# Kernel tuning notes

Hardware: AMD Instinct MI355X
Metric: run time of the kernel (lower is better)

The kernel has to match this reference:

```python
import jax, jax.numpy as jnp
import numpy as np

B, T, D, M, HID = 8, 128, 512, 2048, 128
EPS = 1e-5

def layer_norm(x, g, b):
    mu = jnp.mean(x, axis=-1, keepdims=True)
    var = jnp.mean((x - mu) ** 2, axis=-1, keepdims=True)
    return (x - mu) * jax.lax.rsqrt(var + EPS) * g + b

def setup_inputs() -> dict:
    key = jax.random.key(0)
    ks = jax.random.split(key, 12)
    f32 = jnp.float32
    inp = {
        'e': jax.random.normal(ks[0], (B, T, D), f32),
        'h': jax.random.randint(ks[1], (D,), 0, M),
        'sign': (jax.random.randint(ks[2], (D,), 0, 2) * 2 - 1).astype(f32),
        'Wq': jax.random.normal(ks[3], (D, D), f32) / np.sqrt(D),
        'Wk': jax.random.normal(ks[4], (D, D), f32) / np.sqrt(D),
        'Wv': jax.random.normal(ks[5], (D, D), f32) / np.sqrt(D),
        'ro_w1': jax.random.normal(ks[6], (M, HID), f32) / np.sqrt(M),
        'ro_b1': jnp.zeros((HID,), f32),
        'ro_w2': jax.random.normal(ks[7], (HID, D), f32) / np.sqrt(HID),
        'ro_b2': jnp.zeros((D,), f32),
        'vp_ln_g': jnp.ones((D,), f32),
        'vp_ln_b': jnp.zeros((D,), f32),
        'vp_w1': jax.random.normal(ks[8], (D, D), f32) / np.sqrt(D),
        'vp_b1': jnp.zeros((D,), f32),
        'vp_w2': jax.random.normal(ks[9], (D, D), f32) / np.sqrt(D),
        'vp_b2': jnp.zeros((D,), f32),
        'ln_g': jnp.ones((D,), f32),
        'ln_b': jnp.zeros((D,), f32),
        'theta_q_raw': jnp.asarray(0.05, f32),
        'theta_k_raw': jnp.asarray(0.05, f32),
        'omega_raw': jnp.asarray(0.02, f32),
        'gate_feat_raw': jnp.asarray(-2.5, f32),
        'gate_val_raw': jnp.asarray(-2.5, f32),
    }
    return inp

def reference(e, h, sign, Wq, Wk, Wv, ro_w1, ro_b1, ro_w2, ro_b2,
              vp_ln_g, vp_ln_b, vp_w1, vp_b1, vp_w2, vp_b2, ln_g, ln_b,
              theta_q_raw, theta_k_raw, omega_raw, gate_feat_raw, gate_val_raw):
    sg = jax.lax.stop_gradient
    # CountSketch as a sparse signed projection matrix (d -> m), row i hits col h[i].
    CS = jnp.zeros((D, M), e.dtype).at[jnp.arange(D), h].set(sign)
    theta_q = 0.5 * jnp.tanh(theta_q_raw)
    theta_k = 0.5 * jnp.tanh(theta_k_raw)
    omega = 0.5 * jnp.tanh(omega_raw)
    g_feat = 0.25 * jax.nn.sigmoid(gate_feat_raw)  # gate_cap_feat=0.25
    g_val = 0.25 * jax.nn.sigmoid(gate_val_raw)    # gate_cap_val=0.25

    def step(carry, xs):
        K, H = carry              # K:(B,2,M)  H:(B,2,D,M)  (detached buffers)
        e_t, t = xs               # e_t:(B,D)  t: scalar position
        pos = jnp.full((e_t.shape[0], 1), t, e_t.dtype)
        q = e_t @ Wq
        k = e_t @ Wk
        v = e_t @ Wv
        ph_q = theta_q * q - omega * pos
        ph_k = theta_k * k + omega * pos
        Q_re = (q * jnp.cos(ph_q)) @ CS
        Q_im = (q * jnp.sin(ph_q)) @ CS
        dK_re = (k * jnp.cos(ph_k)) @ CS
        dK_im = (k * jnp.sin(ph_k)) @ CS
        # FFT polynomial convolution of query sketch with prefix-key sketch
        FQ = jnp.fft.fft(jax.lax.complex(Q_re, Q_im), norm='ortho')
        Kd = sg(K)
        FK = jnp.fft.fft(jax.lax.complex(Kd[:, 0, :], Kd[:, 1, :]), norm='ortho')
        tscale = jnp.sqrt(pos + 1.0)
        psi = jnp.fft.ifft(FQ * FK, norm='ortho').real / tscale
        h_feat = jax.nn.gelu(psi @ ro_w1 + ro_b1, approximate=False) @ ro_w2 + ro_b2
        # value readout against prefix H (reads are detached, as in torch)
        Hd = sg(H)
        vread = (jnp.einsum('bdm,bm->bd', Hd[:, 0], sg(Q_re))
                 - jnp.einsum('bdm,bm->bd', Hd[:, 1], sg(Q_im))) / tscale
        vread = layer_norm(vread, vp_ln_g, vp_ln_b)
        vread = jax.nn.gelu(vread @ vp_w1 + vp_b1, approximate=False) @ vp_w2 + vp_b2
        y = layer_norm(e_t + g_feat * h_feat + g_val * vread, ln_g, ln_b)
        dK = sg(jnp.stack([dK_re, dK_im], axis=1))        # (B,2,M)
        K_next = Kd + dK
        H_next = Hd + v[:, None, :, None] * dK[:, :, None, :]
        return (K_next, H_next), y

    K0 = jnp.zeros((B, 2, M), e.dtype)
    H0 = jnp.zeros((B, 2, D, M), e.dtype)
    pos_seq = jnp.arange(T, dtype=e.dtype)
    (Kf, Hf), ys = jax.lax.scan(step, (K0, H0), (jnp.transpose(e, (1, 0, 2)), pos_seq))
    return jnp.transpose(ys, (1, 0, 2)), Kf, Hf
```

## Files before the change

kernel.cpp:

```cpp
#include <hip/hip_runtime.h>
#include <hip/hip_bf16.h>
#include <math.h>

#define B_   8
#define T_   128
#define D_   512
#define M_   2048
#define HID_ 128
#define BT_  1024

typedef __attribute__((ext_vector_type(8))) short short8t;
typedef __attribute__((ext_vector_type(8))) unsigned short ushort8t;
typedef __attribute__((ext_vector_type(4))) unsigned short ushort4t;
typedef __attribute__((ext_vector_type(4))) float f32x4;
typedef __hip_bfloat16 bf16;

#define OFF_SCAL   0L
#define OFF_QKV    16L
#define OFF_KP     (OFF_QKV + 1572864L)
#define OFF_VRAW   (OFF_KP + 2097152L)
#define OFF_VF     (OFF_VRAW + 524288L)
#define OFF_HFEAT  (OFF_VF + 524288L)
#define OFF_EB     (OFF_HFEAT + 524288L)
#define OFF_WQKVT  (OFF_EB + 262144L)
#define OFF_VP1T   (OFF_WQKVT + 393216L)
#define OFF_VP2T   (OFF_VP1T + 131072L)
#define OFF_RO2T   (OFF_VP2T + 131072L)
#define OFF_QCAT   (OFF_RO2T + 32768L)
#define OFF_KCAT   (OFF_QCAT + 2097152L)
#define OFF_DKT    (OFF_KCAT + 2097152L)
#define OFF_VTB    (OFF_DKT + 2097152L)
#define OFF_VLNB   (OFF_VTB + 262144L)
#define OFF_V1B    (OFF_VLNB + 262144L)
#define OFF_SCOA   (OFF_V1B + 262144L)
#define OFF_QSUM   (OFF_SCOA + 131072L)
#define OFF_PCAT   (OFF_QSUM + 131072L)
#define OFF_RO1F   (OFF_PCAT + 2097152L)
#define OFF_HACC   (OFF_RO1F + 262144L)

#define FLAG_BIAS     1
#define FLAG_GELU     2
#define FLAG_ROWSCALE 4
#define FLAG_ATOMIC   8
#define FLAG_HFB      32
#define FLAG_TRI      64

__device__ __forceinline__ float gelu_f(float x) {
    return 0.5f * x * (1.0f + erff(x * 0.70710678118654752440f));
}

__device__ __forceinline__ float b2f(unsigned short u) {
    return __uint_as_float(((unsigned int)u) << 16);
}

#define PIDX(i) ((i) + ((i) >> 5))

template<int M>
__device__ __forceinline__ void dif_one(float* re, float* im, int tid) {
    #pragma unroll
    for (int u = 0; u < 4; ++u) {
        int q = u * 256 + tid;
        int k = q & (M - 1);
        int i = (q / M) * (2 * M) + k;
        float s, c;
        __sincosf((float)k * (3.14159265358979323846f / (float)M), &s, &c);
        int p0 = PIDX(i), p1 = PIDX(i + M);
        float ar = re[p0], ai = im[p0], br = re[p1], bi = im[p1];
        re[p0] = ar + br; im[p0] = ai + bi;
        float dr = ar - br, di = ai - bi;
        re[p1] = dr * c + di * s;
        im[p1] = di * c - dr * s;
    }
}

__global__ __launch_bounds__(256) void preproc_kernel(
    const float* tq, const float* tk, const float* om, const float* gf, const float* gv,
    float* scal, float* scoacc, float* hacc,
    const float4* __restrict__ e4, ushort4t* __restrict__ eb4,
    const float* w0, const float* w1, const float* w2, const float* w3,
    const float* w4, const float* w5,
    bf16* d0, bf16* d1, bf16* d2, bf16* d3, bf16* d4, bf16* d5,
    const float* __restrict__ ro_w1, bf16* __restrict__ ro1f)
{
    __shared__ float smem[4224];
    int blk = blockIdx.x, tid = threadIdx.x;

    if (blk < 1024) {
        int idx = blk * 256 + tid;
        if (idx < 131072) scoacc[idx] = 0.f;
        else hacc[idx - 131072] = 0.f;
        if (idx == 0) {
            scal[0] = 0.5f * tanhf(tq[0]);
            scal[1] = 0.5f * tanhf(tk[0]);
            scal[2] = 0.5f * tanhf(om[0]);
            scal[3] = 0.25f / (1.0f + expf(-gf[0]));
            scal[4] = 0.25f / (1.0f + expf(-gv[0]));
        }
        return;
    }
    if (blk < 1536) {
        int i = (blk - 1024) * 256 + tid;
        float4 v = e4[i];
        ushort4t o;
        bf16 h0 = __float2bfloat16(v.x), h1 = __float2bfloat16(v.y);
        bf16 h2 = __float2bfloat16(v.z), h3 = __float2bfloat16(v.w);
        o[0] = *(unsigned short*)&h0; o[1] = *(unsigned short*)&h1;
        o[2] = *(unsigned short*)&h2; o[3] = *(unsigned short*)&h3;
        eb4[i] = o;
        return;
    }
    if (blk < 3072) {
        int zz = blk - 1536;
        int wz = zz >> 8;
        int rem = zz & 255;
        int by = rem >> 4, bx = rem & 15;
        const float* src; bf16* dst; int R = 512;
        if (wz == 0)      { src = w0; dst = d0; }
        else if (wz == 1) { src = w1; dst = d1; }
        else if (wz == 2) { src = w2; dst = d2; }
        else if (wz == 3) { src = w3; dst = d3; }
        else if (wz == 4) { src = w4; dst = d4; }
        else              { src = w5; dst = d5; R = 128; }
        int c0 = bx * 32, r0 = by * 32;
        if (r0 >= R) return;
        float (*tile)[33] = (float(*)[33])smem;
        int tx = tid & 31, ty = tid >> 5;
        for (int rr = ty; rr < 32; rr += 8) {
            int r = r0 + rr;
            tile[rr][tx] = (r < R) ? src[(long)r * 512 + c0 + tx] : 0.f;
        }
        __syncthreads();
        int r = r0 + tx;
        if (r < R)
            for (int cc = ty; cc < 32; cc += 8)
                dst[(long)(c0 + cc) * R + r] = __float2bfloat16(tile[tx][cc]);
        return;
    }
    {
        int j = blk - 3072;
        float* Rs = smem;
        float* Is = smem + 2112;
        for (int u = 0; u < 8; ++u) {
            int n = u * 256 + tid;
            Rs[PIDX(n)] = ro_w1[(long)n * HID_ + j];
            Is[PIDX(n)] = 0.f;
        }
        __syncthreads();
#define FSTEP(MM) dif_one<MM>(Rs, Is, tid); __syncthreads();
        FSTEP(1024) FSTEP(512) FSTEP(256) FSTEP(128) FSTEP(64)
        FSTEP(32) FSTEP(16) FSTEP(8) FSTEP(4) FSTEP(2) FSTEP(1)
#undef FSTEP
        unsigned short* op = (unsigned short*)(ro1f + (long)j * 4096);
        for (int u = 0; u < 8; ++u) {
            int r = u * 256 + tid;
            int pr = PIDX(r);
            bf16 re = __float2bfloat16(Rs[pr]);
            bf16 im = __float2bfloat16(Is[pr]);
            op[r]        = *(unsigned short*)&re;
            op[2048 + r] = *(unsigned short*)&im;
        }
    }
}

__global__ __launch_bounds__(256) void sketchvtb_kernel(const float* __restrict__ qkv,
                                                        const float* __restrict__ sign,
                                                        const float* __restrict__ scal,
                                                        const int* __restrict__ h,
                                                        bf16* __restrict__ qcat,
                                                        bf16* __restrict__ kcat,
                                                        bf16* __restrict__ vTb) {
    __shared__ float smem[4 * M_];
    int blk = blockIdx.x, tid = threadIdx.x;
    if (blk < 1024) {
        int bt = blk;
        float* s0 = smem;
        float* s1 = smem + M_;
        float* s2 = smem + 2 * M_;
        float* s3 = smem + 3 * M_;
        for (int j = tid; j < M_; j += 256) { s0[j] = 0.f; s1[j] = 0.f; s2[j] = 0.f; s3[j] = 0.f; }
        __syncthreads();
        int t = bt & 127;
        float thq = scal[0], thk = scal[1], omg = scal[2];
        float ft = (float)t;
        for (int i = tid; i < D_; i += 256) {
            float q = qkv[(long)bt * 1536 + i];
            float k = qkv[(long)bt * 1536 + 512 + i];
            float sg = sign[i];
            float sq_, cq_, sk_, ck_;
            __sincosf(thq * q - omg * ft, &sq_, &cq_);
            __sincosf(thk * k + omg * ft, &sk_, &ck_);
            int m = h[i];
            atomicAdd(&s0[m], q * cq_ * sg);
            atomicAdd(&s1[m], q * sq_ * sg);
            atomicAdd(&s2[m], k * ck_ * sg);
            atomicAdd(&s3[m], k * sk_ * sg);
        }
        __syncthreads();
        long qb = (long)bt * 4096;
        for (int j = tid; j < M_; j += 256) {
            qcat[qb + j]        = __float2bfloat16(s0[j]);
            qcat[qb + 2048 + j] = __float2bfloat16(s1[j]);
            kcat[qb + j]        = __float2bfloat16(s2[j]);
            kcat[qb + 2048 + j] = __float2bfloat16(-s3[j]);
        }
        return;
    }
    {
        int zz = blk - 1024;
        int b = zz >> 6;
        int rem = zz & 63;
        int by = rem >> 4, bx = rem & 15;
        int c0 = bx * 32, r0 = by * 32;
        float (*tile)[33] = (float(*)[33])smem;
        int tx = tid & 31, ty = tid >> 5;
        const float* in = qkv + 1024 + (long)b * 196608L;
        for (int rr = ty; rr < 32; rr += 8)
            tile[rr][tx] = in[(long)(r0 + rr) * 1536 + c0 + tx];
        __syncthreads();
        bf16* out = vTb + (long)b * 65536L;
        for (int cc = ty; cc < 32; cc += 8)
            out[(long)(c0 + cc) * 128 + r0 + tx] = __float2bfloat16(tile[tx][cc]);
    }
}

__global__ __launch_bounds__(256) void prefix_p1(const bf16* __restrict__ kcat,
                                                 float* __restrict__ qsum) {
    int idx = blockIdx.x * 256 + threadIdx.x;
    int col = idx & 32767, q = idx >> 15;
    int m = col & 2047, b = (col >> 11) & 7, comp = col >> 14;
    const unsigned short* src = (const unsigned short*)kcat
        + ((long)(b * 128 + q * 32) * 4096L + (long)comp * 2048L + m);
    float s = 0.f;
    #pragma unroll 8
    for (int i = 0; i < 32; ++i) s += b2f(src[(long)i * 4096L]);
    if (comp) s = -s;
    qsum[(long)q * 32768 + col] = s;
}

__global__ __launch_bounds__(256) void prefix_p2(const bf16* __restrict__ kcat,
                                                 const float* __restrict__ qsum,
                                                 bf16* __restrict__ KP16,
                                                 bf16* __restrict__ dkT,
                                                 float* __restrict__ kf_out) {
    int idx = blockIdx.x * 256 + threadIdx.x;
    int col = idx & 32767, q = idx >> 15;
    int m = col & 2047, b = (col >> 11) & 7, comp = col >> 14;
    const unsigned short* src = (const unsigned short*)kcat
        + ((long)(b * 128 + q * 32) * 4096L + (long)comp * 2048L + m);
    bf16* dst = KP16 + (long)comp * BT_ * M_ + (long)b * T_ * M_ + m + (long)(q * 32) * M_;
    bf16* dkt = dkT + (long)comp * 2097152L + (long)b * 262144L + (long)m * 128L + (long)(q * 32);
    float acc = 0.f;
    for (int p = 0; p < q; ++p) acc += qsum[(long)p * 32768 + col];
    float sgn = comp ? -1.f : 1.f;
    #pragma unroll 4
    for (int i = 0; i < 32; ++i) {
        float v = sgn * b2f(src[(long)i * 4096L]);
        dst[(long)i * M_] = __float2bfloat16(acc);
        dkt[i] = __float2bfloat16(v);
        acc += v;
    }
    if (q == 3) kf_out[((long)b * 2 + comp) * M_ + m] = acc;
}

template<int S>
__device__ __forceinline__ void dif8_pair(float* r0, float* i0a, float* r1, float* i1a, int tid) {
    int k = tid % S;
    int grp = tid / S;
    int base = grp * 8 * S + k;
    float sw, cw;
    __sincosf((float)k * (3.14159265358979323846f / (4.0f * (float)S)), &sw, &cw);
    float wr = cw, wi = -sw;
    float w2r = wr * wr - wi * wi, w2i = 2.f * wr * wi;
    float w4r = w2r * w2r - w2i * w2i, w4i = 2.f * w2r * w2i;
    const float RH = 0.70710678118654752440f;
    float t1r[4] = {wr, (wr + wi) * RH, wi, (wi - wr) * RH};
    float t1i[4] = {wi, (wi - wr) * RH, -wr, -(wr + wi) * RH};
    float u0r = w2r, u0i = w2i;
    float u1r = w2i, u1i = -w2r;
    #pragma unroll
    for (int a = 0; a < 2; ++a) {
        float* re = a ? r1 : r0;
        float* im = a ? i1a : i0a;
        float xr[8], xi[8];
        #pragma unroll
        for (int r = 0; r < 8; ++r) { int p = PIDX(base + r * S); xr[r] = re[p]; xi[r] = im[p]; }
        #pragma unroll
        for (int r = 0; r < 4; ++r) {
            float ar = xr[r], ai = xi[r], br = xr[r + 4], bi = xi[r + 4];
            xr[r] = ar + br; xi[r] = ai + bi;
            float dr = ar - br, di = ai - bi;
            xr[r + 4] = dr * t1r[r] - di * t1i[r];
            xi[r + 4] = dr * t1i[r] + di * t1r[r];
        }
        #pragma unroll
        for (int hb = 0; hb < 8; hb += 4) {
            #pragma unroll
            for (int r = 0; r < 2; ++r) {
                float tr = (r == 0) ? u0r : u1r, ti = (r == 0) ? u0i : u1i;
                float ar = xr[hb + r], ai = xi[hb + r], br = xr[hb + r + 2], bi = xi[hb + r + 2];
                xr[hb + r] = ar + br; xi[hb + r] = ai + bi;
                float dr = ar - br, di = ai - bi;
                xr[hb + r + 2] = dr * tr - di * ti;
                xi[hb + r + 2] = dr * ti + di * tr;
            }
        }
        #pragma unroll
        for (int r = 0; r < 8; r += 2) {
            float ar = xr[r], ai = xi[r], br = xr[r + 1], bi = xi[r + 1];
            xr[r] = ar + br; xi[r] = ai + bi;
            float dr = ar - br, di = ai - bi;
            xr[r + 1] = dr * w4r - di * w4i;
            xi[r + 1] = dr * w4i + di * w4r;
        }
        #pragma unroll
        for (int r = 0; r < 8; ++r) { int p = PIDX(base + r * S); re[p] = xr[r]; im[p] = xi[r]; }
    }
}

#define GEMM_CORE(ABASE, BBASE, KK)                                            \
    for (int kt = k0; kt < k0 + klen; kt += 32) {                              \
        *(float4*)&As[lrow][lk] = *(const float4*)&(ABASE)[(long)lrow * (KK) + kt + lk]; \
        *(float4*)&Bs[lrow][lk] = *(const float4*)&(BBASE)[(long)lrow * (KK) + kt + lk]; \
        __syncthreads();                                                       \
        short8t a0 = *(const short8t*)&As[wr + fm][fk];                        \
        short8t a1 = *(const short8t*)&As[wr + 16 + fm][fk];                   \
        short8t b0 = *(const short8t*)&Bs[wc + fm][fk];                        \
        short8t b1 = *(const short8t*)&Bs[wc + 16 + fm][fk];                   \
        acc00 = __builtin_amdgcn_mfma_f32_16x16x32_bf16(a0, b0, acc00, 0, 0, 0); \
        acc01 = __builtin_amdgcn_mfma_f32_16x16x32_bf16(a0, b1, acc01, 0, 0, 0); \
        acc10 = __builtin_amdgcn_mfma_f32_16x16x32_bf16(a1, b0, acc10, 0, 0, 0); \
        acc11 = __builtin_amdgcn_mfma_f32_16x16x32_bf16(a1, b1, acc11, 0, 0, 0); \
        __syncthreads();                                                       \
    }

__global__ __launch_bounds__(256) void fftsco_kernel(const bf16* __restrict__ qcat,
                                                     const bf16* __restrict__ KP16,
                                                     bf16* __restrict__ pcat,
                                                     const bf16* __restrict__ kcat,
                                                     float* __restrict__ scoacc) {
    __shared__ float smem[8448];
    int blk = blockIdx.x, tid = threadIdx.x;

    if (blk >= 1024) {
        int s = blk - 1024;
        int xx = s % 3, bz = s / 3;
        int tby = (xx > 0) ? 1 : 0, tbx = (xx == 2) ? 1 : 0;
        int batch = bz >> 4, kslice = bz & 15;
        const int K = 4096;
        int klen = 256, k0 = kslice * 256;
        bf16 (*As)[44] = (bf16(*)[44])smem;
        bf16 (*Bs)[44] = (bf16(*)[44])(smem + 1408);
        const bf16* Ab = qcat + (long)batch * 524288L + (long)tby * 64 * K;
        const bf16* Bb = kcat + (long)batch * 524288L + (long)tbx * 64 * K;
        int lrow = tid >> 2, lk = (tid & 3) * 8;
        int w = tid >> 6, lane = tid & 63;
        int wr = (w >> 1) * 32, wc = (w & 1) * 32;
        int fm = lane & 15, fk = (lane >> 4) * 8;
        f32x4 acc00 = {0.f,0.f,0.f,0.f}, acc01 = acc00, acc10 = acc00, acc11 = acc00;
        GEMM_CORE(Ab, Bb, K)
        float* Cf = scoacc + (long)batch * 16384L;
        int row_base = tby * 64 + wr + (lane >> 4) * 4;
        int col_base = tbx * 64 + wc + fm;
        #pragma unroll
        for (int fr = 0; fr < 2; ++fr)
            #pragma unroll
            for (int fc = 0; fc < 2; ++fc) {
                const f32x4& a = fr == 0 ? (fc == 0 ? acc00 : acc01) : (fc == 0 ? acc10 : acc11);
                #pragma unroll
                for (int r = 0; r < 4; ++r)
                    atomicAdd(&Cf[(long)(row_base + fr * 16 + r) * 128 + col_base + fc * 16], a[r]);
            }
        return;
    }

    float* KRs = smem;
    float* KIs = smem + 2112;
    float* QRs = smem + 4224;
    float* QIs = smem + 6336;
    int bt = blk;
    const unsigned short* qp = (const unsigned short*)(qcat + (long)bt * 4096);
    const unsigned short* kpr = (const unsigned short*)(KP16 + (long)bt * M_);
    const unsigned short* kpi = (const unsigned short*)(KP16 + (long)BT_ * M_ + (long)bt * M_);
    for (int u = 0; u < 8; ++u) {
        int j = u * 256 + tid;
        int pj = PIDX(j);
        KRs[pj] = b2f(kpr[j]);
        KIs[pj] = b2f(kpi[j]);
        QRs[pj] = b2f(qp[j]);
        QIs[pj] = b2f(qp[2048 + j]);
    }
    __syncthreads();
    dif8_pair<256>(KRs, KIs, QRs, QIs, tid);  __syncthreads();
    dif8_pair<32>(KRs, KIs, QRs, QIs, tid);   __syncthreads();

    float kr_[8], ki_[8], qr_[8], qi_[8];
    #pragma unroll
    for (int l = 0; l < 8; ++l) {
        int pj = PIDX(8 * tid + l);
        kr_[l] = KRs[pj]; ki_[l] = KIs[pj];
        qr_[l] = QRs[pj]; qi_[l] = QIs[pj];
    }

    const float C16[16] = {1.f, 0.98078528f, 0.92387953f, 0.83146961f,
                           0.70710678f, 0.55557023f, 0.38268343f, 0.19509032f,
                           0.f, -0.19509032f, -0.38268343f, -0.55557023f,
                           -0.70710678f, -0.83146961f, -0.92387953f, -0.98078528f};
    const float S16[16] = {0.f, 0.19509032f, 0.38268343f, 0.55557023f,
                           0.70710678f, 0.83146961f, 0.92387953f, 0.98078528f,
                           1.f, 0.98078528f, 0.92387953f, 0.83146961f,
                           0.70710678f, 0.55557023f, 0.38268343f, 0.19509032f};
    bool odd = (tid & 1) != 0;
    {
        bool hi2 = (tid & 2) != 0;
        #pragma unroll
        for (int l = 0; l < 8; ++l) {
            float c = odd ? C16[l + 8] : C16[l];
            float s = odd ? S16[l + 8] : S16[l];
            float pr, pi2, sr, si, dr, di;
            pr = __shfl_xor(kr_[l], 2); pi2 = __shfl_xor(ki_[l], 2);
            sr = kr_[l] + pr; si = ki_[l] + pi2;
            dr = pr - kr_[l]; di = pi2 - ki_[l];
            kr_[l] = hi2 ? (dr * c + di * s) : sr;
            ki_[l] = hi2 ? (di * c - dr * s) : si;
            pr = __shfl_xor(qr_[l], 2); pi2 = __shfl_xor(qi_[l], 2);
            sr = qr_[l] + pr; si = qi_[l] + pi2;
            dr = pr - qr_[l]; di = pi2 - qi_[l];
            qr_[l] = hi2 ? (dr * c + di * s) : sr;
            qi_[l] = hi2 ? (di * c - dr * s) : si;
        }
    }
    {
        #pragma unroll
        for (int l = 0; l < 8; ++l) {
            float c = C16[2 * l];
            float s = S16[2 * l];
            float pr, pi2, sr, si, dr, di;
            pr = __shfl_xor(kr_[l], 1); pi2 = __shfl_xor(ki_[l], 1);
            sr = kr_[l] + pr; si = ki_[l] + pi2;
            dr = pr - kr_[l]; di = pi2 - ki_[l];
            kr_[l] = odd ? (dr * c + di * s) : sr;
            ki_[l] = odd ? (di * c - dr * s) : si;
            pr = __shfl_xor(qr_[l], 1); pi2 = __shfl_xor(qi_[l], 1);
            sr = qr_[l] + pr; si = qi_[l] + pi2;
            dr = pr - qr_[l]; di = pi2 - qi_[l];
            qr_[l] = odd ? (dr * c + di * s) : sr;
            qi_[l] = odd ? (di * c - dr * s) : si;
        }
    }
    {
        const float C4[4] = {1.f, 0.70710678f, 0.f, -0.70710678f};
        const float S4[4] = {0.f, 0.70710678f, 1.f, 0.70710678f};
        #pragma unroll
        for (int l = 0; l < 4; ++l) {
            float ar, ai, br, bi, dr, di;
            ar = kr_[l]; ai = ki_[l]; br = kr_[l + 4]; bi = ki_[l + 4];
            kr_[l] = ar + br; ki_[l] = ai + bi;
            dr = ar - br; di = ai - bi;
            kr_[l + 4] = dr * C4[l] + di * S4[l];
            ki_[l + 4] = di * C4[l] - dr * S4[l];
            ar = qr_[l]; ai = qi_[l]; br = qr_[l + 4]; bi = qi_[l + 4];
            qr_[l] = ar + br; qi_[l] = ai + bi;
            dr = ar - br; di = ai - bi;
            qr_[l + 4] = dr * C4[l] + di * S4[l];
            qi_[l + 4] = di * C4[l] - dr * S4[l];
        }
    }
    #pragma unroll
    for (int b2 = 0; b2 < 8; b2 += 4) {
        {
            float ar = kr_[b2], ai = ki_[b2], br = kr_[b2 + 2], bi = ki_[b2 + 2];
            kr_[b2] = ar + br; ki_[b2] = ai + bi;
            kr_[b2 + 2] = ar - br; ki_[b2 + 2] = ai - bi;
            ar = qr_[b2]; ai = qi_[b2]; br = qr_[b2 + 2]; bi = qi_[b2 + 2];
            qr_[b2] = ar + br; qi_[b2] = ai + bi;
            qr_[b2 + 2] = ar - br; qi_[b2 + 2] = ai - bi;
        }
        {
            float ar = kr_[b2 + 1], ai = ki_[b2 + 1], br = kr_[b2 + 3], bi = ki_[b2 + 3];
            kr_[b2 + 1] = ar + br; ki_[b2 + 1] = ai + bi;
            float dr = ar - br, di = ai - bi;
            kr_[b2 + 3] = di; ki_[b2 + 3] = -dr;
            ar = qr_[b2 + 1]; ai = qi_[b2 + 1]; br = qr_[b2 + 3]; bi = qi_[b2 + 3];
            qr_[b2 + 1] = ar + br; qi_[b2 + 1] = ai + bi;
            dr = ar - br; di = ai - bi;
            qr_[b2 + 3] = di; qi_[b2 + 3] = -dr;
        }
    }
    #pragma unroll
    for (int i0 = 0; i0 < 8; i0 += 2) {
        float ar = kr_[i0], ai = ki_[i0], br = kr_[i0 + 1], bi = ki_[i0 + 1];
        kr_[i0] = ar + br; ki_[i0] = ai + bi;
        kr_[i0 + 1] = ar - br; ki_[i0 + 1] = ai - bi;
        ar = qr_[i0]; ai = qi_[i0]; br = qr_[i0 + 1]; bi = qi_[i0 + 1];
        qr_[i0] = ar + br; qi_[i0] = ai + bi;
        qr_[i0 + 1] = ar - br; qi_[i0 + 1] = ai - bi;
    }

    unsigned short* op = (unsigned short*)(pcat + (long)bt * 4096 + 8 * tid);
    ushort8t ore, oim;
    #pragma unroll
    for (int l = 0; l < 8; ++l) {
        float pr = qr_[l] * kr_[l] - qi_[l] * ki_[l];
        float pi2 = qr_[l] * ki_[l] + qi_[l] * kr_[l];
        bf16 hr = __float2bfloat16(pr);
        bf16 hi = __float2bfloat16(pi2);
        ore[l] = *(unsigned short*)&hr;
        oim[l] = *(unsigned short*)&hi;
    }
    *(ushort8t*)op = ore;
    *(ushort8t*)(op + 2048) = oim;
}

__global__ __launch_bounds__(256) void v1hid_kernel(const bf16* __restrict__ vlnb,
                                                    const bf16* __restrict__ vp1T,
                                                    const float* __restrict__ vp_b1,
                                                    bf16* __restrict__ v1b,
                                                    const bf16* __restrict__ pcat,
                                                    const bf16* __restrict__ ro1f,
                                                    float* __restrict__ hacc) {
    __shared__ __align__(16) bf16 As[64][44];
    __shared__ __align__(16) bf16 Bs[64][44];
    int blk = blockIdx.x, tid = threadIdx.x;
    int lrow = tid >> 2, lk = (tid & 3) * 8;
    int w = tid >> 6, lane = tid & 63;
    int wr = (w >> 1) * 32, wc = (w & 1) * 32;
    int fm = lane & 15, fk = (lane >> 4) * 8;
    f32x4 acc00 = {0.f,0.f,0.f,0.f}, acc01 = acc00, acc10 = acc00, acc11 = acc00;

    if (blk < 128) {
        int tbx = blk & 7, tby = blk >> 3;
        const int K = 512;
        int klen = K, k0 = 0;
        const bf16* Ab = vlnb + (long)tby * 64 * K;
        const bf16* Bb = vp1T + (long)tbx * 64 * K;
        GEMM_CORE(Ab, Bb, K)
        int row_base = tby * 64 + wr + (lane >> 4) * 4;
        int col_base = tbx * 64 + wc + fm;
        #pragma unroll
        for (int fr = 0; fr < 2; ++fr)
            #pragma unroll
            for (int fc = 0; fc < 2; ++fc) {
                const f32x4& a = fr == 0 ? (fc == 0 ? acc00 : acc01) : (fc == 0 ? acc10 : acc11);
                #pragma unroll
                for (int r = 0; r < 4; ++r) {
                    int gi = row_base + fr * 16 + r, gj = col_base + fc * 16;
                    v1b[(long)gi * 512 + gj] = __float2bfloat16(gelu_f(a[r] + vp_b1[gj]));
                }
            }
        return;
    }
    {
        int s2 = blk - 128;
        int tbx = s2 & 1, tby = (s2 >> 1) & 15, kslice = s2 >> 5;
        const int K = 4096;
        int klen = 512, k0 = kslice * 512;
        const bf16* Ab = pcat + (long)tby * 64 * K;
        const bf16* Bb = ro1f + (long)tbx * 64 * K;
        GEMM_CORE(Ab, Bb, K)
        int row_base = tby * 64 + wr + (lane >> 4) * 4;
        int col_base = tbx * 64 + wc + fm;
        #pragma unroll
        for (int fr = 0; fr < 2; ++fr)
            #pragma unroll
            for (int fc = 0; fc < 2; ++fc) {
                const f32x4& a = fr == 0 ? (fc == 0 ? acc00 : acc01) : (fc == 0 ? acc10 : acc11);
                #pragma unroll
                for (int r = 0; r < 4; ++r)
                    atomicAdd(&hacc[(long)(row_base + fr * 16 + r) * 128 + col_base + fc * 16], a[r]);
            }
    }
}

template<int FLAGS, int OUTB16, int AMODE>
__global__ __launch_bounds__(256) void gemm_mfma(
    const void* __restrict__ Av, const bf16* __restrict__ Bt,
    const float* __restrict__ bias, const float* __restrict__ abias,
    void* __restrict__ Cv,
    int K, int ldc, long abz, long bbz, long cbz, int splitk)
{
    __shared__ __align__(16) bf16 As[64][44];
    __shared__ __align__(16) bf16 Bs[64][44];
    int bz = blockIdx.z;
    int batch = bz, kslice = 0;
    if (FLAGS & FLAG_ATOMIC) { batch = bz / splitk; kslice = bz % splitk; }
    int tbx = blockIdx.x, tby = blockIdx.y;
    long aoff;
    const bf16* Bb;
    long coff;
    if (FLAGS & FLAG_HFB) {
        int b = bz & 7, c = bz >> 3;
        aoff = (long)b * abz + (long)tby * 64 * K;
        Bb = Bt + (long)c * 2097152L + (long)b * 262144L + (long)tbx * 64 * K;
        coff = (long)b * 2097152L + (long)c * 1048576L;
    } else {
        aoff = (long)batch * abz + (long)tby * 64 * K;
        Bb = Bt + (long)batch * bbz + (long)tbx * 64 * K;
        coff = (long)batch * cbz;
    }
    int tid = threadIdx.x;
    int lrow = tid >> 2;
    int lk = (tid & 3) * 8;
    int w = tid >> 6, lane = tid & 63;
    int wr = (w >> 1) * 32, wc = (w & 1) * 32;
    int fm = lane & 15, fk = (lane >> 4) * 8;
    f32x4 acc00 = {0.f,0.f,0.f,0.f}, acc01 = acc00, acc10 = acc00, acc11 = acc00;

    int klen = K / splitk;
    int k0 = kslice * klen;
    for (int kt = k0; kt < k0 + klen; kt += 32) {
        if (AMODE == 0) {
            const bf16* Ab = (const bf16*)Av + aoff;
            *(float4*)&As[lrow][lk] = *(const float4*)&Ab[(long)lrow * K + kt + lk];
        } else {
            const float* Af = (const float*)Av + aoff;
            int gk0 = kt + lk;
            float4 v0 = *(const float4*)&Af[(long)lrow * K + gk0];
            float4 v1 = *(const float4*)&Af[(long)lrow * K + gk0 + 4];
            float vv[8] = {v0.x, v0.y, v0.z, v0.w, v1.x, v1.y, v1.z, v1.w};
            int grow = tby * 64 + lrow;
            #pragma unroll
            for (int j = 0; j < 8; ++j) {
                float val = vv[j];
                int gk = gk0 + j;
                if (AMODE == 1) val = (gk < grow) ? val : 0.f;
                As[lrow][lk + j] = __float2bfloat16(val);
            }
        }
        *(float4*)&Bs[lrow][lk] = *(const float4*)&Bb[(long)lrow * K + kt + lk];
        __syncthreads();
        short8t a0 = *(const short8t*)&As[wr + fm][fk];
        short8t a1 = *(const short8t*)&As[wr + 16 + fm][fk];
        short8t b0 = *(const short8t*)&Bs[wc + fm][fk];
        short8t b1 = *(const short8t*)&Bs[wc + 16 + fm][fk];
        acc00 = __builtin_amdgcn_mfma_f32_16x16x32_bf16(a0, b0, acc00, 0, 0, 0);
        acc01 = __builtin_amdgcn_mfma_f32_16x16x32_bf16(a0, b1, acc01, 0, 0, 0);
        acc10 = __builtin_amdgcn_mfma_f32_16x16x32_bf16(a1, b0, acc10, 0, 0, 0);
        acc11 = __builtin_amdgcn_mfma_f32_16x16x32_bf16(a1, b1, acc11, 0, 0, 0);
        __syncthreads();
    }

    float* Cf = (float*)Cv;
    bf16* Cb = (bf16*)Cv;
    int row_base = tby * 64 + wr + (lane >> 4) * 4;
    int col_base = tbx * 64 + wc + fm;
    #pragma unroll
    for (int fr = 0; fr < 2; ++fr) {
        #pragma unroll
        for (int fc = 0; fc < 2; ++fc) {
            const f32x4& a = fr == 0 ? (fc == 0 ? acc00 : acc01) : (fc == 0 ? acc10 : acc11);
            #pragma unroll
            for (int r = 0; r < 4; ++r) {
                int gi = row_base + fr * 16 + r;
                int gj = col_base + fc * 16;
                float v = a[r];
                long ci = coff + (long)gi * ldc + gj;
                if (FLAGS & FLAG_ATOMIC) {
                    atomicAdd(&Cf[ci], v);
                } else {
                    if (FLAGS & FLAG_BIAS) v += bias[gj];
                    if (FLAGS & FLAG_GELU) v = gelu_f(v);
                    if (FLAGS & FLAG_ROWSCALE) v *= rsqrtf((float)(gi & 127) + 1.0f);
                    if (OUTB16) Cb[ci] = __float2bfloat16(v);
                    else        Cf[ci] = v;
                }
            }
        }
    }
}

__global__ __launch_bounds__(256) void gemm_dual(
    const bf16* __restrict__ v1b, const bf16* __restrict__ vp2T, const float* __restrict__ vp_b2,
    const float* __restrict__ hacc, const bf16* __restrict__ ro2T, const float* __restrict__ ro_b1,
    const float* __restrict__ ro_b2, float* __restrict__ vf, float* __restrict__ hfeat)
{
    __shared__ __align__(16) bf16 As[64][44];
    __shared__ __align__(16) bf16 Bs[64][44];
    int tid = threadIdx.x;
    int lrow = tid >> 2, lk = (tid & 3) * 8;
    int w = tid >> 6, lane = tid & 63;
    int wr = (w >> 1) * 32, wc = (w & 1) * 32;
    int fm = lane & 15, fk = (lane >> 4) * 8;
    f32x4 acc00 = {0.f,0.f,0.f,0.f}, acc01 = acc00, acc10 = acc00, acc11 = acc00;
    int mode = blockIdx.z;
    int K = mode ? 128 : 512;
    const bf16* Bb = (mode ? ro2T : vp2T) + (long)blockIdx.x * 64 * K;

    for (int kt = 0; kt < K; kt += 32) {
        if (mode == 0) {
            const bf16* Ab = v1b + (long)blockIdx.y * 64 * K;
            *(float4*)&As[lrow][lk] = *(const float4*)&Ab[(long)lrow * K + kt + lk];
        } else {
            const float* Af = hacc + (long)blockIdx.y * 64 * K;
            int gk0 = kt + lk;
            float4 v0 = *(const float4*)&Af[(long)lrow * K + gk0];
            float4 v1 = *(const float4*)&Af[(long)lrow * K + gk0 + 4];
            float vv[8] = {v0.x, v0.y, v0.z, v0.w, v1.x, v1.y, v1.z, v1.w};
            int grow = blockIdx.y * 64 + lrow;
            float sc = rsqrtf((float)((grow & 127) + 1)) * (1.0f / 92681.900089f);
            #pragma unroll
            for (int j = 0; j < 8; ++j)
                As[lrow][lk + j] = __float2bfloat16(gelu_f(vv[j] * sc + ro_b1[gk0 + j]));
        }
        *(float4*)&Bs[lrow][lk] = *(const float4*)&Bb[(long)lrow * K + kt + lk];
        __syncthreads();
        short8t a0 = *(const short8t*)&As[wr + fm][fk];
        short8t a1 = *(const short8t*)&As[wr + 16 + fm][fk];
        short8t b0 = *(const short8t*)&Bs[wc + fm][fk];
        short8t b1 = *(const short8t*)&Bs[wc + 16 + fm][fk];
        acc00 = __builtin_amdgcn_mfma_f32_16x16x32_bf16(a0, b0, acc00, 0, 0, 0);
        acc01 = __builtin_amdgcn_mfma_f32_16x16x32_bf16(a0, b1, acc01, 0, 0, 0);
        acc10 = __builtin_amdgcn_mfma_f32_16x16x32_bf16(a1, b0, acc10, 0, 0, 0);
        acc11 = __builtin_amdgcn_mfma_f32_16x16x32_bf16(a1, b1, acc11, 0, 0, 0);
        __syncthreads();
    }

    const float* bias = mode ? ro_b2 : vp_b2;
    float* Cf = mode ? hfeat : vf;
    int row_base = blockIdx.y * 64 + wr + (lane >> 4) * 4;
    int col_base = blockIdx.x * 64 + wc + fm;
    #pragma unroll
    for (int fr = 0; fr < 2; ++fr) {
        #pragma unroll
        for (int fc = 0; fc < 2; ++fc) {
            const f32x4& a = fr == 0 ? (fc == 0 ? acc00 : acc01) : (fc == 0 ? acc10 : acc11);
            #pragma unroll
            for (int r = 0; r < 4; ++r) {
                int gi = row_base + fr * 16 + r;
                int gj = col_base + fc * 16;
                Cf[(long)gi * 512 + gj] = a[r] + bias[gj];
            }
        }
    }
}

template<int FINAL, int OB16>
__global__ __launch_bounds__(256) void ln_kernel(const float* __restrict__ x1,
                                                 const float* __restrict__ x2,
                                                 const float* __restrict__ x3,
                                                 const float* __restrict__ g,
                                                 const float* __restrict__ bb,
                                                 const float* __restrict__ scal,
                                                 void* __restrict__ outv) {
    int row = blockIdx.x, tid = threadIdx.x;
    long base = (long)row * D_;
    int d0 = tid, d1 = tid + 256;
    float v0, v1;
    if (FINAL) {
        float gf = scal[3], gv = scal[4];
        v0 = x1[base + d0] + gf * x2[base + d0] + gv * x3[base + d0];
        v1 = x1[base + d1] + gf * x2[base + d1] + gv * x3[base + d1];
    } else {
        v0 = x1[base + d0];
        v1 = x1[base + d1];
    }
    float s = v0 + v1;
    #pragma unroll
    for (int o = 32; o > 0; o >>= 1) s += __shfl_down(s, o);
    __shared__ float red[8];
    int wid = tid >> 6, lane = tid & 63;
    if (lane == 0) red[wid] = s;
    __syncthreads();
    float mu = (red[0] + red[1] + red[2] + red[3]) * (1.0f / D_);
    float e0 = v0 - mu, e1 = v1 - mu;
    float sq = e0 * e0 + e1 * e1;
    #pragma unroll
    for (int o = 32; o > 0; o >>= 1) sq += __shfl_down(sq, o);
    if (lane == 0) red[4 + wid] = sq;
    __syncthreads();
    float var = (red[4] + red[5] + red[6] + red[7]) * (1.0f / D_);
    float rs = rsqrtf(var + 1e-5f);
    float o0 = e0 * rs * g[d0] + bb[d0];
    float o1 = e1 * rs * g[d1] + bb[d1];
    if (OB16) {
        ((bf16*)outv)[base + d0] = __float2bfloat16(o0);
        ((bf16*)outv)[base + d1] = __float2bfloat16(o1);
    } else {
        ((float*)outv)[base + d0] = o0;
        ((float*)outv)[base + d1] = o1;
    }
}

extern "C" void kernel_launch(void* const* d_in, const int* in_sizes, int n_in,
                              void* d_out, int out_size, void* d_ws, size_t ws_size,
                              hipStream_t stream) {
    const float* e      = (const float*)d_in[0];
    const int*   h      = (const int*)d_in[1];
    const float* sign   = (const float*)d_in[2];
    const float* Wq     = (const float*)d_in[3];
    const float* Wk     = (const float*)d_in[4];
    const float* Wv     = (const float*)d_in[5];
    const float* ro_w1  = (const float*)d_in[6];
    const float* ro_b1  = (const float*)d_in[7];
    const float* ro_w2  = (const float*)d_in[8];
    const float* ro_b2  = (const float*)d_in[9];
    const float* vp_ln_g= (const float*)d_in[10];
    const float* vp_ln_b= (const float*)d_in[11];
    const float* vp_w1  = (const float*)d_in[12];
    const float* vp_b1  = (const float*)d_in[13];
    const float* vp_w2  = (const float*)d_in[14];
    const float* vp_b2  = (const float*)d_in[15];
    const float* ln_g   = (const float*)d_in[16];
    const float* ln_b   = (const float*)d_in[17];
    const float* tq     = (const float*)d_in[18];
    const float* tk     = (const float*)d_in[19];
    const float* om     = (const float*)d_in[20];
    const float* gfr    = (const float*)d_in[21];
    const float* gvr    = (const float*)d_in[22];

    float* ws    = (float*)d_ws;
    float* scal  = ws + OFF_SCAL;
    float* qkv   = ws + OFF_QKV;
    float* vraw  = ws + OFF_VRAW;
    float* vf    = ws + OFF_VF;
    float* hfeat = ws + OFF_HFEAT;
    float* scoacc= ws + OFF_SCOA;
    float* qsum  = ws + OFF_QSUM;
    float* hacc  = ws + OFF_HACC;
    bf16* kp16  = (bf16*)(ws + OFF_KP);
    bf16* eb    = (bf16*)(ws + OFF_EB);
    bf16* wqkvT = (bf16*)(ws + OFF_WQKVT);
    bf16* vp1T  = (bf16*)(ws + OFF_VP1T);
    bf16* vp2T  = (bf16*)(ws + OFF_VP2T);
    bf16* ro2T  = (bf16*)(ws + OFF_RO2T);
    bf16* qcat  = (bf16*)(ws + OFF_QCAT);
    bf16* kcat  = (bf16*)(ws + OFF_KCAT);
    bf16* dkT   = (bf16*)(ws + OFF_DKT);
    bf16* vTb   = (bf16*)(ws + OFF_VTB);
    bf16* vlnb  = (bf16*)(ws + OFF_VLNB);
    bf16* v1b   = (bf16*)(ws + OFF_V1B);
    bf16* pcat  = (bf16*)(ws + OFF_PCAT);
    bf16* ro1f  = (bf16*)(ws + OFF_RO1F);

    float* ys = (float*)d_out;
    float* kf = ys + (long)BT_ * D_;
    float* hf = kf + (long)B_ * 2 * M_;

    preproc_kernel<<<3200, 256, 0, stream>>>(
        tq, tk, om, gfr, gvr, scal, scoacc, hacc,
        (const float4*)e, (ushort4t*)eb,
        Wq, Wk, Wv, vp_w1, vp_w2, ro_w2,
        wqkvT, wqkvT + 262144, wqkvT + 524288, vp1T, vp2T, ro2T,
        ro_w1, ro1f);

    gemm_mfma<0, 0, 0><<<dim3(24, 16, 1), 256, 0, stream>>>(
        eb, wqkvT, nullptr, nullptr, qkv, 512, 1536, 0, 0, 0, 1);

    sketchvtb_kernel<<<1536, 256, 0, stream>>>(qkv, sign, scal, h, qcat, kcat, vTb);

    prefix_p1<<<512, 256, 0, stream>>>(kcat, qsum);
    prefix_p2<<<512, 256, 0, stream>>>(kcat, qsum, kp16, dkT, kf);

    fftsco_kernel<<<1408, 256, 0, stream>>>(qcat, kp16, pcat, kcat, scoacc);

    gemm_mfma<FLAG_ROWSCALE, 0, 1><<<dim3(8, 2, 8), 256, 0, stream>>>(
        scoacc, vTb, nullptr, nullptr, vraw, 128, 512, 16384, 65536, 65536, 1);

    ln_kernel<0, 1><<<1024, 256, 0, stream>>>(vraw, nullptr, nullptr, vp_ln_g, vp_ln_b, scal, vlnb);

    v1hid_kernel<<<384, 256, 0, stream>>>(vlnb, vp1T, vp_b1, v1b, pcat, ro1f, hacc);

    gemm_dual<<<dim3(8, 16, 2), 256, 0, stream>>>(
        v1b, vp2T, vp_b2, hacc, ro2T, ro_b1, ro_b2, vf, hfeat);

    ln_kernel<1, 0><<<1024, 256, 0, stream>>>(e, hfeat, vf, ln_g, ln_b, scal, ys);

    gemm_mfma<FLAG_HFB, 0, 0><<<dim3(32, 8, 16), 256, 0, stream>>>(
        vTb, dkT, nullptr, nullptr, hf, 128, 2048, 65536, 0, 0, 1);
}
```

Baseline: 131.9 us.

## Fuse final H-state GEMM into the FFT/score kernel launch as extra blocks

```diff
diff --git a/kernel.cpp b/kernel.cpp
--- a/kernel.cpp
+++ b/kernel.cpp
@@ -42,8 +42,6 @@
 #define FLAG_GELU     2
 #define FLAG_ROWSCALE 4
 #define FLAG_ATOMIC   8
-#define FLAG_HFB      32
-#define FLAG_TRI      64
 
 __device__ __forceinline__ float gelu_f(float x) {
     return 0.5f * x * (1.0f + erff(x * 0.70710678118654752440f));
@@ -333,13 +331,47 @@
         __syncthreads();                                                       \
     }
 
-__global__ __launch_bounds__(256) void fftsco_kernel(const bf16* __restrict__ qcat,
-                                                     const bf16* __restrict__ KP16,
-                                                     bf16* __restrict__ pcat,
-                                                     const bf16* __restrict__ kcat,
-                                                     float* __restrict__ scoacc) {
+__global__ __launch_bounds__(256) void fftscohf_kernel(const bf16* __restrict__ qcat,
+                                                       const bf16* __restrict__ KP16,
+                                                       bf16* __restrict__ pcat,
+                                                       const bf16* __restrict__ kcat,
+                                                       float* __restrict__ scoacc,
+                                                       const bf16* __restrict__ vTb,
+                                                       const bf16* __restrict__ dkT,
+                                                       float* __restrict__ hf) {
     __shared__ float smem[8448];
     int blk = blockIdx.x, tid = threadIdx.x;
+
+    if (blk >= 1408) {
+        int zz = blk - 1408;
+        int tbx = zz & 31, tby = (zz >> 5) & 7, bz = zz >> 8;
+        int b = bz & 7, c = bz >> 3;
+        const int K = 128;
+        int klen = 128, k0 = 0;
+        bf16 (*As)[44] = (bf16(*)[44])smem;
+        bf16 (*Bs)[44] = (bf16(*)[44])(smem + 1408);
+        const bf16* Ab = vTb + (long)b * 65536L + (long)tby * 64 * K;
+        const bf16* Bb = dkT + (long)c * 2097152L + (long)b * 262144L + (long)tbx * 64 * K;
+        int lrow = tid >> 2, lk = (tid & 3) * 8;
+        int w = tid >> 6, lane = tid & 63;
+        int wr = (w >> 1) * 32, wc = (w & 1) * 32;
+        int fm = lane & 15, fk = (lane >> 4) * 8;
+        f32x4 acc00 = {0.f,0.f,0.f,0.f}, acc01 = acc00, acc10 = acc00, acc11 = acc00;
+        GEMM_CORE(Ab, Bb, K)
+        float* Cf = hf + (long)b * 2097152L + (long)c * 1048576L;
+        int row_base = tby * 64 + wr + (lane >> 4) * 4;
+        int col_base = tbx * 64 + wc + fm;
+        #pragma unroll
+        for (int fr = 0; fr < 2; ++fr)
+            #pragma unroll
+            for (int fc = 0; fc < 2; ++fc) {
+                const f32x4& a = fr == 0 ? (fc == 0 ? acc00 : acc01) : (fc == 0 ? acc10 : acc11);
+                #pragma unroll
+                for (int r = 0; r < 4; ++r)
+                    Cf[(long)(row_base + fr * 16 + r) * 2048 + col_base + fc * 16] = a[r];
+            }
+        return;
+    }
 
     if (blk >= 1024) {
         int s = blk - 1024;
@@ -584,19 +616,9 @@
     int batch = bz, kslice = 0;
     if (FLAGS & FLAG_ATOMIC) { batch = bz / splitk; kslice = bz % splitk; }
     int tbx = blockIdx.x, tby = blockIdx.y;
-    long aoff;
-    const bf16* Bb;
-    long coff;
-    if (FLAGS & FLAG_HFB) {
-        int b = bz & 7, c = bz >> 3;
-        aoff = (long)b * abz + (long)tby * 64 * K;
-        Bb = Bt + (long)c * 2097152L + (long)b * 262144L + (long)tbx * 64 * K;
-        coff = (long)b * 2097152L + (long)c * 1048576L;
-    } else {
-        aoff = (long)batch * abz + (long)tby * 64 * K;
-        Bb = Bt + (long)batch * bbz + (long)tbx * 64 * K;
-        coff = (long)batch * cbz;
-    }
+    long aoff = (long)batch * abz + (long)tby * 64 * K;
+    const bf16* Bb = Bt + (long)batch * bbz + (long)tbx * 64 * K;
+    long coff = (long)batch * cbz;
     int tid = threadIdx.x;
     int lrow = tid >> 2;
     int lk = (tid & 3) * 8;
@@ -850,7 +872,7 @@
     prefix_p1<<<512, 256, 0, stream>>>(kcat, qsum);
     prefix_p2<<<512, 256, 0, stream>>>(kcat, qsum, kp16, dkT, kf);
 
-    fftsco_kernel<<<1408, 256, 0, stream>>>(qcat, kp16, pcat, kcat, scoacc);
+    fftscohf_kernel<<<5504, 256, 0, stream>>>(qcat, kp16, pcat, kcat, scoacc, vTb, dkT, hf);
 
     gemm_mfma<FLAG_ROWSCALE, 0, 1><<<dim3(8, 2, 8), 256, 0, stream>>>(
         scoacc, vTb, nullptr, nullptr, vraw, 128, 512, 16384, 65536, 65536, 1);
@@ -863,7 +885,4 @@
         v1b, vp2T, vp_b2, hacc, ro2T, ro_b1, ro_b2, vf, hfeat);
 
     ln_kernel<1, 0><<<1024, 256, 0, stream>>>(e, hfeat, vf, ln_g, ln_b, scal, ys);
-
-    gemm_mfma<FLAG_HFB, 0, 0><<<dim3(32, 8, 16), 256, 0, stream>>>(
-        vTb, dkT, nullptr, nullptr, hf, 128, 2048, 65536, 0, 0, 1);
-}
+}
```

Result: slower. 152.9 us (+15.9%).
